# Kernel tuning notes

Measured on AMD Instinct MI355X. Metric: run time of the kernel, lower is better.

Reference implementation:

```python
import jax, jax.numpy as jnp
import numpy as np
from jax.ops import segment_sum


def gcn_conv(x, edge_index, W, b):
    """PyG GCNConv: add self-loops, symmetric D^-1/2 (A+I) D^-1/2 normalization,
    then aggregate normalized messages at target nodes. edge_weight=None -> ones."""
    N = x.shape[0]
    loops = jnp.arange(N, dtype=edge_index.dtype)
    row = jnp.concatenate([edge_index[0], loops])  # source nodes
    col = jnp.concatenate([edge_index[1], loops])  # target nodes
    w = jnp.ones(row.shape[0], dtype=x.dtype)
    deg = segment_sum(w, col, num_segments=N)
    dinv = jnp.where(deg > 0, jax.lax.rsqrt(deg), 0.0)
    norm = dinv[row] * dinv[col]                    # [E+N]
    xw = x @ W                                      # dense transform [N, out]
    msg = xw[row] * norm[:, None]                   # gather + scale [E+N, out]
    out = segment_sum(msg, col, num_segments=N)     # scatter-add at targets
    return out + b


def setup_inputs() -> dict:
    key = jax.random.key(0)
    k1, k2, k3, k4 = jax.random.split(key, 4)
    N, E, nhid, nfeat = 50000, 800000, 256, 128
    x = jax.random.normal(k1, (N, nhid), dtype=jnp.float32)
    edge_index = jax.random.randint(k2, (2, E), 0, N, dtype=jnp.int64)
    W1 = jax.random.normal(k3, (nhid, nhid), dtype=jnp.float32) * (1.0 / np.sqrt(nhid))
    b1 = jnp.zeros((nhid,), dtype=jnp.float32)
    W2 = jax.random.normal(k4, (nhid, nfeat), dtype=jnp.float32) * (1.0 / np.sqrt(nhid))
    b2 = jnp.zeros((nfeat,), dtype=jnp.float32)
    return {"x": x, "edge_index": edge_index, "W1": W1, "b1": b1, "W2": W2, "b2": b2}


def reference(x, edge_index, W1, b1, W2, b2):
    h = jax.nn.relu(gcn_conv(x, edge_index, W1, b1))
    # dropout is identity in eval mode (deterministic reference)
    return gcn_conv(h, edge_index, W2, b2)
```

## Files before the change

### kernel.cpp

```cpp
#include <hip/hip_runtime.h>
#include <math.h>


typedef _Float16 h8 __attribute__((ext_vector_type(8)));
typedef float    f32x4 __attribute__((ext_vector_type(4)));

#define CAP 64

__global__ void k_zero(int* __restrict__ deg, int* __restrict__ govf, int N) {
    int i = blockIdx.x * blockDim.x + threadIdx.x;
    if (i < N) deg[i] = 0;
    if (i == 0) *govf = 0;
}

template<bool A32>
__device__ __forceinline__ void gemm_body(
    const float* __restrict__ X32, const _Float16* __restrict__ X16,
    const _Float16* __restrict__ Wt, _Float16* __restrict__ Y,
    int M, int K, int NC, int bx, int by)
{
    __shared__ _Float16 As[128][40];
    __shared__ _Float16 Bs[128][40];

    const int bn = bx * 128;
    const int bm = by * 128;
    const int tid = threadIdx.x;
    const int w = tid >> 6, l = tid & 63;
    const int wm = (w >> 1) * 64, wn = (w & 1) * 64;
    const int lr = l & 15, lg = l >> 4;

    const int arow = tid >> 2, acol = (tid & 3) * 8;
    const int xrow = tid >> 1, xcol = (tid & 1) * 16;

    f32x4 acc[4][4];
    #pragma unroll
    for (int i = 0; i < 4; i++)
        #pragma unroll
        for (int j = 0; j < 4; j++)
            acc[i][j] = (f32x4){0.f, 0.f, 0.f, 0.f};

    float4 pf0, pf1, pf2, pf3;
    h8 pa0, pa1;
    h8 pb0, pb1;

    auto loadA = [&](int k0) {
        if (A32) {
            int gm0 = bm + arow;      if (gm0 >= M) gm0 = M - 1;
            int gm1 = bm + 64 + arow; if (gm1 >= M) gm1 = M - 1;
            pf0 = *reinterpret_cast<const float4*>(&X32[(long)gm0 * K + k0 + acol]);
            pf1 = *reinterpret_cast<const float4*>(&X32[(long)gm0 * K + k0 + acol + 4]);
            pf2 = *reinterpret_cast<const float4*>(&X32[(long)gm1 * K + k0 + acol]);
            pf3 = *reinterpret_cast<const float4*>(&X32[(long)gm1 * K + k0 + acol + 4]);
        } else {
            int gm = bm + xrow; if (gm >= M) gm = M - 1;
            pa0 = *reinterpret_cast<const h8*>(&X16[(long)gm * K + k0 + xcol]);
            pa1 = *reinterpret_cast<const h8*>(&X16[(long)gm * K + k0 + xcol + 8]);
        }
    };
    auto loadB = [&](int k0) {
        pb0 = *reinterpret_cast<const h8*>(&Wt[(long)(bn + xrow) * K + k0 + xcol]);
        pb1 = *reinterpret_cast<const h8*>(&Wt[(long)(bn + xrow) * K + k0 + xcol + 8]);
    };

    loadA(0); loadB(0);
    for (int k0 = 0; k0 < K; k0 += 32) {
        if (A32) {
            h8 h0, h1;
            h0[0] = (_Float16)pf0.x; h0[1] = (_Float16)pf0.y;
            h0[2] = (_Float16)pf0.z; h0[3] = (_Float16)pf0.w;
            h0[4] = (_Float16)pf1.x; h0[5] = (_Float16)pf1.y;
            h0[6] = (_Float16)pf1.z; h0[7] = (_Float16)pf1.w;
            h1[0] = (_Float16)pf2.x; h1[1] = (_Float16)pf2.y;
            h1[2] = (_Float16)pf2.z; h1[3] = (_Float16)pf2.w;
            h1[4] = (_Float16)pf3.x; h1[5] = (_Float16)pf3.y;
            h1[6] = (_Float16)pf3.z; h1[7] = (_Float16)pf3.w;
            *reinterpret_cast<h8*>(&As[arow][acol]) = h0;
            *reinterpret_cast<h8*>(&As[64 + arow][acol]) = h1;
        } else {
            *reinterpret_cast<h8*>(&As[xrow][xcol]) = pa0;
            *reinterpret_cast<h8*>(&As[xrow][xcol + 8]) = pa1;
        }
        *reinterpret_cast<h8*>(&Bs[xrow][xcol]) = pb0;
        *reinterpret_cast<h8*>(&Bs[xrow][xcol + 8]) = pb1;
        __syncthreads();

        if (k0 + 32 < K) { loadA(k0 + 32); loadB(k0 + 32); }

        h8 a[4], b[4];
        #pragma unroll
        for (int i = 0; i < 4; i++)
            a[i] = *reinterpret_cast<const h8*>(&As[wm + i * 16 + lr][lg * 8]);
        #pragma unroll
        for (int j = 0; j < 4; j++)
            b[j] = *reinterpret_cast<const h8*>(&Bs[wn + j * 16 + lr][lg * 8]);
        #pragma unroll
        for (int i = 0; i < 4; i++)
            #pragma unroll
            for (int j = 0; j < 4; j++)
                acc[i][j] = __builtin_amdgcn_mfma_f32_16x16x32_f16(
                    a[i], b[j], acc[i][j], 0, 0, 0);
        __syncthreads();
    }

    #pragma unroll
    for (int i = 0; i < 4; i++) {
        #pragma unroll
        for (int r = 0; r < 4; r++) {
            int gm = bm + wm + i * 16 + lg * 4 + r;
            if (gm < M) {
                #pragma unroll
                for (int j = 0; j < 4; j++)
                    Y[(long)gm * NC + bn + wn + j * 16 + lr] =
                        (_Float16)acc[i][j][r];
            }
        }
    }
}

__global__ __launch_bounds__(256) void k_count_prep(
    const int* __restrict__ col, int E, int* __restrict__ deg, int* __restrict__ rank,
    int ncb,
    const float* __restrict__ W1, const float* __restrict__ W2,
    _Float16* __restrict__ wt1, _Float16* __restrict__ wt2,
    int K, int n1, int n2)
{
    if ((int)blockIdx.x < ncb) {
        int i = blockIdx.x * blockDim.x + threadIdx.x;
        int s = ncb * blockDim.x;
        for (int e = i; e < E; e += s) rank[e] = atomicAdd(&deg[col[e]], 1);
        return;
    }
    int i = (blockIdx.x - ncb) * blockDim.x + threadIdx.x;
    int c1 = K * n1;
    if (i < c1) {
        int k = i / n1, n = i % n1;
        wt1[(long)n * K + k] = (_Float16)W1[i];
    } else if (i < c1 + K * n2) {
        int j = i - c1;
        int k = j / n2, n = j % n2;
        wt2[(long)n * K + k] = (_Float16)W2[j];
    }
}

__global__ __launch_bounds__(256) void k_gemm_fill(
    const float* __restrict__ X32, const _Float16* __restrict__ Wt,
    _Float16* __restrict__ Y, int M, int K, int NC, int ngb, int gx,
    const int* __restrict__ row, const int* __restrict__ col,
    const int* __restrict__ rank, int E,
    const int* __restrict__ deg, float* __restrict__ dinv, int N,
    int* __restrict__ srcidx, int2* __restrict__ ovf, int* __restrict__ govf,
    int zb)
{
    if ((int)blockIdx.x < ngb) {
        int gb = blockIdx.x;
        gemm_body<true>(X32, nullptr, Wt, Y, M, K, NC, gb % gx, gb / gx);
        return;
    }
    if ((int)blockIdx.x < ngb + zb) {
        int i = (blockIdx.x - ngb) * blockDim.x + threadIdx.x;
        if (i < N) dinv[i] = rsqrtf(1.f + (float)deg[i]);
        return;
    }
    int g = (blockIdx.x - ngb - zb) * blockDim.x + threadIdx.x;
    int nthreads = (gridDim.x - ngb - zb) * blockDim.x;
    if ((E & 3) == 0) {
        int G4 = E >> 2;
        for (int q = g; q < G4; q += nthreads) {
            int e = q << 2;
            int4 c4 = *reinterpret_cast<const int4*>(&col[e]);
            int4 r4 = *reinterpret_cast<const int4*>(&row[e]);
            int4 k4 = *reinterpret_cast<const int4*>(&rank[e]);
            if (k4.x < CAP) srcidx[c4.x * CAP + k4.x] = r4.x;
            else { int o = atomicAdd(govf, 1); ovf[o] = make_int2(r4.x, c4.x); }
            if (k4.y < CAP) srcidx[c4.y * CAP + k4.y] = r4.y;
            else { int o = atomicAdd(govf, 1); ovf[o] = make_int2(r4.y, c4.y); }
            if (k4.z < CAP) srcidx[c4.z * CAP + k4.z] = r4.z;
            else { int o = atomicAdd(govf, 1); ovf[o] = make_int2(r4.z, c4.z); }
            if (k4.w < CAP) srcidx[c4.w * CAP + k4.w] = r4.w;
            else { int o = atomicAdd(govf, 1); ovf[o] = make_int2(r4.w, c4.w); }
        }
    } else {
        for (int e = g; e < E; e += nthreads) {
            int c = col[e], r = row[e], k = rank[e];
            if (k < CAP) srcidx[c * CAP + k] = r;
            else { int o = atomicAdd(govf, 1); ovf[o] = make_int2(r, c); }
        }
    }
}

__global__ __launch_bounds__(256) void k_gemm16(
    const _Float16* __restrict__ X16, const _Float16* __restrict__ Wt,
    _Float16* __restrict__ Y, int M, int K, int NC)
{
    gemm_body<false>(nullptr, X16, Wt, Y, M, K, NC, blockIdx.x, blockIdx.y);
}

template<bool F16OUT, bool RELU>
__global__ __launch_bounds__(256) void k_agg(
    const int* __restrict__ deg, const float* __restrict__ dinv,
    const int* __restrict__ srcidx,
    const int2* __restrict__ ovf, const int* __restrict__ govf,
    const _Float16* __restrict__ Y, const float* __restrict__ bias,
    int N, int FT, int fo,
    float* __restrict__ out32, _Float16* __restrict__ out16)
{
    int node = blockIdx.x * 4 + (threadIdx.x >> 6);
    if (node >= N) return;
    int lane = threadIdx.x & 63;
    int sub = lane >> 4;
    int fl  = lane & 15;
    const int fcol = fo + fl * 8;

    float dc = dinv[node];
    int cnt = min(deg[node], CAP);
    const int beg = node * CAP;

    float acc[8];
    if (sub == 0) {
        h8 v = *reinterpret_cast<const h8*>(&Y[(long)node * FT + fcol]);
        #pragma unroll
        for (int j = 0; j < 8; j++) acc[j] = dc * (float)v[j];
    } else {
        #pragma unroll
        for (int j = 0; j < 8; j++) acc[j] = 0.f;
    }

    int base16 = cnt & ~15;
    for (int i = sub * 4; i < base16; i += 16) {
        int4 r4 = *reinterpret_cast<const int4*>(&srcidx[beg + i]);
        float d0 = dinv[r4.x], d1 = dinv[r4.y], d2 = dinv[r4.z], d3 = dinv[r4.w];
        h8 v0 = *reinterpret_cast<const h8*>(&Y[(long)r4.x * FT + fcol]);
        h8 v1 = *reinterpret_cast<const h8*>(&Y[(long)r4.y * FT + fcol]);
        h8 v2 = *reinterpret_cast<const h8*>(&Y[(long)r4.z * FT + fcol]);
        h8 v3 = *reinterpret_cast<const h8*>(&Y[(long)r4.w * FT + fcol]);
        #pragma unroll
        for (int j = 0; j < 8; j++) {
            acc[j] = fmaf(d0, (float)v0[j], acc[j]);
            acc[j] = fmaf(d1, (float)v1[j], acc[j]);
            acc[j] = fmaf(d2, (float)v2[j], acc[j]);
            acc[j] = fmaf(d3, (float)v3[j], acc[j]);
        }
    }
    for (int i = base16 + sub; i < cnt; i += 4) {
        int r = srcidx[beg + i];
        float d = dinv[r];
        h8 v = *reinterpret_cast<const h8*>(&Y[(long)r * FT + fcol]);
        #pragma unroll
        for (int j = 0; j < 8; j++) acc[j] = fmaf(d, (float)v[j], acc[j]);
    }
    {
        int no = *govf;
        for (int t = sub; t < no; t += 4) {
            int2 pr = ovf[t];
            if (pr.y == node) {
                float d = dinv[pr.x];
                h8 v = *reinterpret_cast<const h8*>(&Y[(long)pr.x * FT + fcol]);
                #pragma unroll
                for (int j = 0; j < 8; j++) acc[j] = fmaf(d, (float)v[j], acc[j]);
            }
        }
    }

    #pragma unroll
    for (int m = 16; m < 64; m <<= 1)
        #pragma unroll
        for (int j = 0; j < 8; j++)
            acc[j] += __shfl_xor(acc[j], m, 64);

    const float4* b4 = reinterpret_cast<const float4*>(&bias[fcol]);
    float4 blo = b4[0], bhi = b4[1];
    float r8[8];
    r8[0] = fmaf(dc, acc[0], blo.x); r8[1] = fmaf(dc, acc[1], blo.y);
    r8[2] = fmaf(dc, acc[2], blo.z); r8[3] = fmaf(dc, acc[3], blo.w);
    r8[4] = fmaf(dc, acc[4], bhi.x); r8[5] = fmaf(dc, acc[5], bhi.y);
    r8[6] = fmaf(dc, acc[6], bhi.z); r8[7] = fmaf(dc, acc[7], bhi.w);
    if (RELU) {
        #pragma unroll
        for (int j = 0; j < 8; j++) r8[j] = fmaxf(r8[j], 0.f);
    }

    long base = (long)node * FT + fcol;
    if (F16OUT) {
        if (sub == 0) {
            h8 o;
            #pragma unroll
            for (int j = 0; j < 8; j++) o[j] = (_Float16)r8[j];
            *reinterpret_cast<h8*>(&out16[base]) = o;
        }
    } else {
        if (sub == 0) {
            *reinterpret_cast<float4*>(&out32[base]) =
                make_float4(r8[0], r8[1], r8[2], r8[3]);
        } else if (sub == 1) {
            *reinterpret_cast<float4*>(&out32[base + 4]) =
                make_float4(r8[4], r8[5], r8[6], r8[7]);
        }
    }
}

extern "C" void kernel_launch(void* const* d_in, const int* in_sizes, int n_in,
                              void* d_out, int out_size, void* d_ws, size_t ws_size,
                              hipStream_t stream)
{
    const float* x   = (const float*)d_in[0];
    const int*   ei  = (const int*)d_in[1];
    const float* W1  = (const float*)d_in[2];
    const float* b1  = (const float*)d_in[3];
    const float* W2  = (const float*)d_in[4];
    const float* b2  = (const float*)d_in[5];

    const int nhid  = in_sizes[3];
    const int nfeat = in_sizes[5];
    const int N     = in_sizes[0] / nhid;
    const int E     = in_sizes[1] / 2;

    const int* row = ei;
    const int* col = ei + E;

    size_t cur = 0;
    auto alloc = [&](size_t bytes) {
        void* p = (char*)d_ws + cur;
        cur += (bytes + 255) & ~(size_t)255;
        return p;
    };
    int*       deg_i  = (int*)alloc((size_t)N * 4);
    int*       govf   = (int*)alloc(256);
    float*     dinv   = (float*)alloc((size_t)N * 4);
    int*       rank   = (int*)alloc((size_t)E * 4);
    int*       srcidx = (int*)alloc((size_t)N * CAP * 4);
    int2*      ovf    = (int2*)alloc((size_t)E * 8);
    _Float16*  wt1    = (_Float16*)alloc((size_t)nhid * nhid * 2);
    _Float16*  wt2    = (_Float16*)alloc((size_t)nhid * nfeat * 2);
    _Float16*  y16    = (_Float16*)alloc((size_t)N * nhid * 2);
    _Float16*  h16    = (_Float16*)alloc((size_t)N * nhid * 2);
    _Float16*  y2     = (_Float16*)alloc((size_t)N * nfeat * 2);
    float*     out    = (float*)d_out;
    (void)ws_size; (void)n_in; (void)out_size;

    const int T = 256;
    const int zb = (N + T - 1) / T;
    const int gx = nhid / 128;
    const int gy = (N + 127) / 128;

    k_zero<<<zb, T, 0, stream>>>(deg_i, govf, N);

    {
        const int ncb = 1024;
        int pb = (nhid * (nhid + nfeat) + T - 1) / T;
        k_count_prep<<<ncb + pb, T, 0, stream>>>(
            col, E, deg_i, rank, ncb, W1, W2, wt1, wt2, nhid, nhid, nfeat);
    }

    {
        int ngb = gx * gy;
        k_gemm_fill<<<ngb + zb + 1024, T, 0, stream>>>(
            x, wt1, y16, N, nhid, nhid, ngb, gx,
            row, col, rank, E, deg_i, dinv, N, srcidx, ovf, govf, zb);
    }

    {
        int nblk = (N + 3) / 4;
        k_agg<true, true><<<nblk, T, 0, stream>>>(
            deg_i, dinv, srcidx, ovf, govf, y16, b1, N, nhid, 0, nullptr, h16);
        k_agg<true, true><<<nblk, T, 0, stream>>>(
            deg_i, dinv, srcidx, ovf, govf, y16, b1, N, nhid, 128, nullptr, h16);
    }

    {
        dim3 grid(nfeat / 128, (N + 127) / 128);
        k_gemm16<<<grid, T, 0, stream>>>(h16, wt2, y2, N, nhid, nfeat);
    }
    {
        int nblk = (N + 3) / 4;
        k_agg<false, false><<<nblk, T, 0, stream>>>(
            deg_i, dinv, srcidx, ovf, govf, y2, b2, N, nfeat, 0, out, nullptr);
    }
}
```

Before: 184.7 us.

## Fuse degree counting into edge fill and drop rank buffer

The atomic degree count and the scatter of source indices into per-node slots now happen in one pass inside the GEMM-combined kernel, so the separate counting pass and the rank array (written and then reread) are gone. Weight conversion is folded into the zeroing kernel, and dinv moves to its own small kernel after the fill. This saves one pass over the column array plus E*4 bytes of rank writes and reads. The cost is one extra kernel launch for dinv, and the fill blocks now wait on atomic return values while they share the GPU with the GEMM.

Result: slower. 189.4 us (+2.5%).

```diff
diff --git a/kernel.cpp b/kernel.cpp
--- a/kernel.cpp
+++ b/kernel.cpp
@@ -7,10 +7,27 @@
 
 #define CAP 64
 
-__global__ void k_zero(int* __restrict__ deg, int* __restrict__ govf, int N) {
-    int i = blockIdx.x * blockDim.x + threadIdx.x;
-    if (i < N) deg[i] = 0;
-    if (i == 0) *govf = 0;
+__global__ void k_zero_prep(int* __restrict__ deg, int* __restrict__ govf, int N,
+                            const float* __restrict__ W1, const float* __restrict__ W2,
+                            _Float16* __restrict__ wt1, _Float16* __restrict__ wt2,
+                            int K, int n1, int n2, int zb)
+{
+    if ((int)blockIdx.x < zb) {
+        int i = blockIdx.x * blockDim.x + threadIdx.x;
+        if (i < N) deg[i] = 0;
+        if (i == 0) *govf = 0;
+    } else {
+        int i = (blockIdx.x - zb) * blockDim.x + threadIdx.x;
+        int c1 = K * n1;
+        if (i < c1) {
+            int k = i / n1, n = i % n1;
+            wt1[(long)n * K + k] = (_Float16)W1[i];
+        } else if (i < c1 + K * n2) {
+            int j = i - c1;
+            int k = j / n2, n = j % n2;
+            wt2[(long)n * K + k] = (_Float16)W2[j];
+        }
+    }
 }
 
 template<bool A32>
@@ -117,75 +134,52 @@
     }
 }
 
-__global__ __launch_bounds__(256) void k_count_prep(
-    const int* __restrict__ col, int E, int* __restrict__ deg, int* __restrict__ rank,
-    int ncb,
-    const float* __restrict__ W1, const float* __restrict__ W2,
-    _Float16* __restrict__ wt1, _Float16* __restrict__ wt2,
-    int K, int n1, int n2)
-{
-    if ((int)blockIdx.x < ncb) {
-        int i = blockIdx.x * blockDim.x + threadIdx.x;
-        int s = ncb * blockDim.x;
-        for (int e = i; e < E; e += s) rank[e] = atomicAdd(&deg[col[e]], 1);
-        return;
-    }
-    int i = (blockIdx.x - ncb) * blockDim.x + threadIdx.x;
-    int c1 = K * n1;
-    if (i < c1) {
-        int k = i / n1, n = i % n1;
-        wt1[(long)n * K + k] = (_Float16)W1[i];
-    } else if (i < c1 + K * n2) {
-        int j = i - c1;
-        int k = j / n2, n = j % n2;
-        wt2[(long)n * K + k] = (_Float16)W2[j];
-    }
-}
-
-__global__ __launch_bounds__(256) void k_gemm_fill(
+__global__ __launch_bounds__(256) void k_gemm_cfg(
     const float* __restrict__ X32, const _Float16* __restrict__ Wt,
     _Float16* __restrict__ Y, int M, int K, int NC, int ngb, int gx,
-    const int* __restrict__ row, const int* __restrict__ col,
-    const int* __restrict__ rank, int E,
-    const int* __restrict__ deg, float* __restrict__ dinv, int N,
-    int* __restrict__ srcidx, int2* __restrict__ ovf, int* __restrict__ govf,
-    int zb)
+    const int* __restrict__ row, const int* __restrict__ col, int E,
+    int* __restrict__ deg, int* __restrict__ srcidx,
+    int2* __restrict__ ovf, int* __restrict__ govf)
 {
     if ((int)blockIdx.x < ngb) {
         int gb = blockIdx.x;
         gemm_body<true>(X32, nullptr, Wt, Y, M, K, NC, gb % gx, gb / gx);
         return;
     }
-    if ((int)blockIdx.x < ngb + zb) {
-        int i = (blockIdx.x - ngb) * blockDim.x + threadIdx.x;
-        if (i < N) dinv[i] = rsqrtf(1.f + (float)deg[i]);
-        return;
-    }
-    int g = (blockIdx.x - ngb - zb) * blockDim.x + threadIdx.x;
-    int nthreads = (gridDim.x - ngb - zb) * blockDim.x;
+    int g = (blockIdx.x - ngb) * blockDim.x + threadIdx.x;
+    int nthreads = (gridDim.x - ngb) * blockDim.x;
     if ((E & 3) == 0) {
         int G4 = E >> 2;
         for (int q = g; q < G4; q += nthreads) {
             int e = q << 2;
             int4 c4 = *reinterpret_cast<const int4*>(&col[e]);
             int4 r4 = *reinterpret_cast<const int4*>(&row[e]);
-            int4 k4 = *reinterpret_cast<const int4*>(&rank[e]);
-            if (k4.x < CAP) srcidx[c4.x * CAP + k4.x] = r4.x;
+            int k0 = atomicAdd(&deg[c4.x], 1);
+            int k1 = atomicAdd(&deg[c4.y], 1);
+            int k2 = atomicAdd(&deg[c4.z], 1);
+            int k3 = atomicAdd(&deg[c4.w], 1);
+            if (k0 < CAP) srcidx[c4.x * CAP + k0] = r4.x;
             else { int o = atomicAdd(govf, 1); ovf[o] = make_int2(r4.x, c4.x); }
-            if (k4.y < CAP) srcidx[c4.y * CAP + k4.y] = r4.y;
+            if (k1 < CAP) srcidx[c4.y * CAP + k1] = r4.y;
             else { int o = atomicAdd(govf, 1); ovf[o] = make_int2(r4.y, c4.y); }
-            if (k4.z < CAP) srcidx[c4.z * CAP + k4.z] = r4.z;
+            if (k2 < CAP) srcidx[c4.z * CAP + k2] = r4.z;
             else { int o = atomicAdd(govf, 1); ovf[o] = make_int2(r4.z, c4.z); }
-            if (k4.w < CAP) srcidx[c4.w * CAP + k4.w] = r4.w;
+            if (k3 < CAP) srcidx[c4.w * CAP + k3] = r4.w;
             else { int o = atomicAdd(govf, 1); ovf[o] = make_int2(r4.w, c4.w); }
         }
     } else {
         for (int e = g; e < E; e += nthreads) {
-            int c = col[e], r = row[e], k = rank[e];
+            int c = col[e], r = row[e];
+            int k = atomicAdd(&deg[c], 1);
             if (k < CAP) srcidx[c * CAP + k] = r;
             else { int o = atomicAdd(govf, 1); ovf[o] = make_int2(r, c); }
         }
     }
+}
+
+__global__ void k_dinv(const int* __restrict__ deg, float* __restrict__ dinv, int N) {
+    int i = blockIdx.x * blockDim.x + threadIdx.x;
+    if (i < N) dinv[i] = rsqrtf(1.f + (float)deg[i]);
 }
 
 __global__ __launch_bounds__(256) void k_gemm16(
@@ -326,7 +320,6 @@
     int*       deg_i  = (int*)alloc((size_t)N * 4);
     int*       govf   = (int*)alloc(256);
     float*     dinv   = (float*)alloc((size_t)N * 4);
-    int*       rank   = (int*)alloc((size_t)E * 4);
     int*       srcidx = (int*)alloc((size_t)N * CAP * 4);
     int2*      ovf    = (int2*)alloc((size_t)E * 8);
     _Float16*  wt1    = (_Float16*)alloc((size_t)nhid * nhid * 2);
@@ -342,21 +335,20 @@
     const int gx = nhid / 128;
     const int gy = (N + 127) / 128;
 
-    k_zero<<<zb, T, 0, stream>>>(deg_i, govf, N);
-
-    {
-        const int ncb = 1024;
+    {
         int pb = (nhid * (nhid + nfeat) + T - 1) / T;
-        k_count_prep<<<ncb + pb, T, 0, stream>>>(
-            col, E, deg_i, rank, ncb, W1, W2, wt1, wt2, nhid, nhid, nfeat);
+        k_zero_prep<<<zb + pb, T, 0, stream>>>(deg_i, govf, N, W1, W2, wt1, wt2,
+                                               nhid, nhid, nfeat, zb);
     }
 
     {
         int ngb = gx * gy;
-        k_gemm_fill<<<ngb + zb + 1024, T, 0, stream>>>(
+        k_gemm_cfg<<<ngb + 1024, T, 0, stream>>>(
             x, wt1, y16, N, nhid, nhid, ngb, gx,
-            row, col, rank, E, deg_i, dinv, N, srcidx, ovf, govf, zb);
-    }
+            row, col, E, deg_i, srcidx, ovf, govf);
+    }
+
+    k_dinv<<<zb, T, 0, stream>>>(deg_i, dinv, N);
 
     {
         int nblk = (N + 3) / 4;
```

## Use full-width 128x256 tiles with 512-thread blocks for first GEMM

Applied to the files above, without the earlier changes.

The first GEMM now gives each 512-thread block a 128x256 output tile covering all output columns, instead of two 128x128 blocks per row tile. Each fp32 row of X is then read and converted to fp16 only once rather than twice, which halves A-side global traffic and conversion work. The fused dinv and fill sections are re-indexed for the 512-thread block size, and the second GEMM is inlined as its own kernel. In exchange, per-block LDS and register use rise, which may lower occupancy, and the fill work runs with the larger block geometry.

New measurement: 177.0 us, median of 2. 4.1% less time.

```diff
diff --git a/kernel.cpp b/kernel.cpp
--- a/kernel.cpp
+++ b/kernel.cpp
@@ -11,110 +11,6 @@
     int i = blockIdx.x * blockDim.x + threadIdx.x;
     if (i < N) deg[i] = 0;
     if (i == 0) *govf = 0;
-}
-
-template<bool A32>
-__device__ __forceinline__ void gemm_body(
-    const float* __restrict__ X32, const _Float16* __restrict__ X16,
-    const _Float16* __restrict__ Wt, _Float16* __restrict__ Y,
-    int M, int K, int NC, int bx, int by)
-{
-    __shared__ _Float16 As[128][40];
-    __shared__ _Float16 Bs[128][40];
-
-    const int bn = bx * 128;
-    const int bm = by * 128;
-    const int tid = threadIdx.x;
-    const int w = tid >> 6, l = tid & 63;
-    const int wm = (w >> 1) * 64, wn = (w & 1) * 64;
-    const int lr = l & 15, lg = l >> 4;
-
-    const int arow = tid >> 2, acol = (tid & 3) * 8;
-    const int xrow = tid >> 1, xcol = (tid & 1) * 16;
-
-    f32x4 acc[4][4];
-    #pragma unroll
-    for (int i = 0; i < 4; i++)
-        #pragma unroll
-        for (int j = 0; j < 4; j++)
-            acc[i][j] = (f32x4){0.f, 0.f, 0.f, 0.f};
-
-    float4 pf0, pf1, pf2, pf3;
-    h8 pa0, pa1;
-    h8 pb0, pb1;
-
-    auto loadA = [&](int k0) {
-        if (A32) {
-            int gm0 = bm + arow;      if (gm0 >= M) gm0 = M - 1;
-            int gm1 = bm + 64 + arow; if (gm1 >= M) gm1 = M - 1;
-            pf0 = *reinterpret_cast<const float4*>(&X32[(long)gm0 * K + k0 + acol]);
-            pf1 = *reinterpret_cast<const float4*>(&X32[(long)gm0 * K + k0 + acol + 4]);
-            pf2 = *reinterpret_cast<const float4*>(&X32[(long)gm1 * K + k0 + acol]);
-            pf3 = *reinterpret_cast<const float4*>(&X32[(long)gm1 * K + k0 + acol + 4]);
-        } else {
-            int gm = bm + xrow; if (gm >= M) gm = M - 1;
-            pa0 = *reinterpret_cast<const h8*>(&X16[(long)gm * K + k0 + xcol]);
-            pa1 = *reinterpret_cast<const h8*>(&X16[(long)gm * K + k0 + xcol + 8]);
-        }
-    };
-    auto loadB = [&](int k0) {
-        pb0 = *reinterpret_cast<const h8*>(&Wt[(long)(bn + xrow) * K + k0 + xcol]);
-        pb1 = *reinterpret_cast<const h8*>(&Wt[(long)(bn + xrow) * K + k0 + xcol + 8]);
-    };
-
-    loadA(0); loadB(0);
-    for (int k0 = 0; k0 < K; k0 += 32) {
-        if (A32) {
-            h8 h0, h1;
-            h0[0] = (_Float16)pf0.x; h0[1] = (_Float16)pf0.y;
-            h0[2] = (_Float16)pf0.z; h0[3] = (_Float16)pf0.w;
-            h0[4] = (_Float16)pf1.x; h0[5] = (_Float16)pf1.y;
-            h0[6] = (_Float16)pf1.z; h0[7] = (_Float16)pf1.w;
-            h1[0] = (_Float16)pf2.x; h1[1] = (_Float16)pf2.y;
-            h1[2] = (_Float16)pf2.z; h1[3] = (_Float16)pf2.w;
-            h1[4] = (_Float16)pf3.x; h1[5] = (_Float16)pf3.y;
-            h1[6] = (_Float16)pf3.z; h1[7] = (_Float16)pf3.w;
-            *reinterpret_cast<h8*>(&As[arow][acol]) = h0;
-            *reinterpret_cast<h8*>(&As[64 + arow][acol]) = h1;
-        } else {
-            *reinterpret_cast<h8*>(&As[xrow][xcol]) = pa0;
-            *reinterpret_cast<h8*>(&As[xrow][xcol + 8]) = pa1;
-        }
-        *reinterpret_cast<h8*>(&Bs[xrow][xcol]) = pb0;
-        *reinterpret_cast<h8*>(&Bs[xrow][xcol + 8]) = pb1;
-        __syncthreads();
-
-        if (k0 + 32 < K) { loadA(k0 + 32); loadB(k0 + 32); }
-
-        h8 a[4], b[4];
-        #pragma unroll
-        for (int i = 0; i < 4; i++)
-            a[i] = *reinterpret_cast<const h8*>(&As[wm + i * 16 + lr][lg * 8]);
-        #pragma unroll
-        for (int j = 0; j < 4; j++)
-            b[j] = *reinterpret_cast<const h8*>(&Bs[wn + j * 16 + lr][lg * 8]);
-        #pragma unroll
-        for (int i = 0; i < 4; i++)
-            #pragma unroll
-            for (int j = 0; j < 4; j++)
-                acc[i][j] = __builtin_amdgcn_mfma_f32_16x16x32_f16(
-                    a[i], b[j], acc[i][j], 0, 0, 0);
-        __syncthreads();
-    }
-
-    #pragma unroll
-    for (int i = 0; i < 4; i++) {
-        #pragma unroll
-        for (int r = 0; r < 4; r++) {
-            int gm = bm + wm + i * 16 + lg * 4 + r;
-            if (gm < M) {
-                #pragma unroll
-                for (int j = 0; j < 4; j++)
-                    Y[(long)gm * NC + bn + wn + j * 16 + lr] =
-                        (_Float16)acc[i][j][r];
-            }
-        }
-    }
 }
 
 __global__ __launch_bounds__(256) void k_count_prep(
@@ -142,27 +38,107 @@
     }
 }
 
-__global__ __launch_bounds__(256) void k_gemm_fill(
+__device__ __forceinline__ void gemm1_body(
     const float* __restrict__ X32, const _Float16* __restrict__ Wt,
-    _Float16* __restrict__ Y, int M, int K, int NC, int ngb, int gx,
+    _Float16* __restrict__ Y, int M, int K, int by)
+{
+    __shared__ _Float16 As[128][40];
+    __shared__ _Float16 Bs[256][40];
+
+    const int bm = by * 128;
+    const int tid = threadIdx.x;
+    const int w = tid >> 6, l = tid & 63;
+    const int wm = (w >> 2) * 64, wn = (w & 3) * 64;
+    const int lr = l & 15, lg = l >> 4;
+
+    const int arow = tid >> 2, acol = (tid & 3) * 8;
+    const int brow = tid >> 1, bcol = (tid & 1) * 16;
+
+    f32x4 acc[4][4];
+    #pragma unroll
+    for (int i = 0; i < 4; i++)
+        #pragma unroll
+        for (int j = 0; j < 4; j++)
+            acc[i][j] = (f32x4){0.f, 0.f, 0.f, 0.f};
+
+    float4 pf0, pf1;
+    h8 pb0, pb1;
+
+    auto loadA = [&](int k0) {
+        int gm = bm + arow; if (gm >= M) gm = M - 1;
+        pf0 = *reinterpret_cast<const float4*>(&X32[(long)gm * K + k0 + acol]);
+        pf1 = *reinterpret_cast<const float4*>(&X32[(long)gm * K + k0 + acol + 4]);
+    };
+    auto loadB = [&](int k0) {
+        pb0 = *reinterpret_cast<const h8*>(&Wt[(long)brow * K + k0 + bcol]);
+        pb1 = *reinterpret_cast<const h8*>(&Wt[(long)brow * K + k0 + bcol + 8]);
+    };
+
+    loadA(0); loadB(0);
+    for (int k0 = 0; k0 < K; k0 += 32) {
+        h8 hv;
+        hv[0] = (_Float16)pf0.x; hv[1] = (_Float16)pf0.y;
+        hv[2] = (_Float16)pf0.z; hv[3] = (_Float16)pf0.w;
+        hv[4] = (_Float16)pf1.x; hv[5] = (_Float16)pf1.y;
+        hv[6] = (_Float16)pf1.z; hv[7] = (_Float16)pf1.w;
+        *reinterpret_cast<h8*>(&As[arow][acol]) = hv;
+        *reinterpret_cast<h8*>(&Bs[brow][bcol]) = pb0;
+        *reinterpret_cast<h8*>(&Bs[brow][bcol + 8]) = pb1;
+        __syncthreads();
+
+        if (k0 + 32 < K) { loadA(k0 + 32); loadB(k0 + 32); }
+
+        h8 a[4], b[4];
+        #pragma unroll
+        for (int i = 0; i < 4; i++)
+            a[i] = *reinterpret_cast<const h8*>(&As[wm + i * 16 + lr][lg * 8]);
+        #pragma unroll
+        for (int j = 0; j < 4; j++)
+            b[j] = *reinterpret_cast<const h8*>(&Bs[wn + j * 16 + lr][lg * 8]);
+        #pragma unroll
+        for (int i = 0; i < 4; i++)
+            #pragma unroll
+            for (int j = 0; j < 4; j++)
+                acc[i][j] = __builtin_amdgcn_mfma_f32_16x16x32_f16(
+                    a[i], b[j], acc[i][j], 0, 0, 0);
+        __syncthreads();
+    }
+
+    #pragma unroll
+    for (int i = 0; i < 4; i++) {
+        #pragma unroll
+        for (int r = 0; r < 4; r++) {
+            int gm = bm + wm + i * 16 + lg * 4 + r;
+            if (gm < M) {
+                #pragma unroll
+                for (int j = 0; j < 4; j++)
+                    Y[(long)gm * 256 + wn + j * 16 + lr] =
+                        (_Float16)acc[i][j][r];
+            }
+        }
+    }
+}
+
+__global__ __launch_bounds__(512) void k_gemm_fill(
+    const float* __restrict__ X32, const _Float16* __restrict__ Wt,
+    _Float16* __restrict__ Y, int M, int K, int ngb,
     const int* __restrict__ row, const int* __restrict__ col,
     const int* __restrict__ rank, int E,
     const int* __restrict__ deg, float* __restrict__ dinv, int N,
     int* __restrict__ srcidx, int2* __restrict__ ovf, int* __restrict__ govf,
-    int zb)
+    int zb5)
 {
     if ((int)blockIdx.x < ngb) {
-        int gb = blockIdx.x;
-        gemm_body<true>(X32, nullptr, Wt, Y, M, K, NC, gb % gx, gb / gx);
+        gemm1_body(X32, Wt, Y, M, K, blockIdx.x);
         return;
     }
-    if ((int)blockIdx.x < ngb + zb) {
+    if ((int)blockIdx.x < ngb + zb5) {
         int i = (blockIdx.x - ngb) * blockDim.x + threadIdx.x;
         if (i < N) dinv[i] = rsqrtf(1.f + (float)deg[i]);
         return;
     }
-    int g = (blockIdx.x - ngb - zb) * blockDim.x + threadIdx.x;
-    int nthreads = (gridDim.x - ngb - zb) * blockDim.x;
+    int g = (blockIdx.x - ngb - zb5) * blockDim.x + threadIdx.x;
+    int nthreads = (gridDim.x - ngb - zb5) * blockDim.x;
     if ((E & 3) == 0) {
         int G4 = E >> 2;
         for (int q = g; q < G4; q += nthreads) {
@@ -192,7 +168,74 @@
     const _Float16* __restrict__ X16, const _Float16* __restrict__ Wt,
     _Float16* __restrict__ Y, int M, int K, int NC)
 {
-    gemm_body<false>(nullptr, X16, Wt, Y, M, K, NC, blockIdx.x, blockIdx.y);
+    __shared__ _Float16 As[128][40];
+    __shared__ _Float16 Bs[128][40];
+
+    const int bn = blockIdx.x * 128;
+    const int bm = blockIdx.y * 128;
+    const int tid = threadIdx.x;
+    const int w = tid >> 6, l = tid & 63;
+    const int wm = (w >> 1) * 64, wn = (w & 1) * 64;
+    const int lr = l & 15, lg = l >> 4;
+    const int xrow = tid >> 1, xcol = (tid & 1) * 16;
+
+    f32x4 acc[4][4];
+    #pragma unroll
+    for (int i = 0; i < 4; i++)
+        #pragma unroll
+        for (int j = 0; j < 4; j++)
+            acc[i][j] = (f32x4){0.f, 0.f, 0.f, 0.f};
+
+    h8 pa0, pa1, pb0, pb1;
+    auto loadA = [&](int k0) {
+        int gm = bm + xrow; if (gm >= M) gm = M - 1;
+        pa0 = *reinterpret_cast<const h8*>(&X16[(long)gm * K + k0 + xcol]);
+        pa1 = *reinterpret_cast<const h8*>(&X16[(long)gm * K + k0 + xcol + 8]);
+    };
+    auto loadB = [&](int k0) {
+        pb0 = *reinterpret_cast<const h8*>(&Wt[(long)(bn + xrow) * K + k0 + xcol]);
+        pb1 = *reinterpret_cast<const h8*>(&Wt[(long)(bn + xrow) * K + k0 + xcol + 8]);
+    };
+
+    loadA(0); loadB(0);
+    for (int k0 = 0; k0 < K; k0 += 32) {
+        *reinterpret_cast<h8*>(&As[xrow][xcol]) = pa0;
+        *reinterpret_cast<h8*>(&As[xrow][xcol + 8]) = pa1;
+        *reinterpret_cast<h8*>(&Bs[xrow][xcol]) = pb0;
+        *reinterpret_cast<h8*>(&Bs[xrow][xcol + 8]) = pb1;
+        __syncthreads();
+
+        if (k0 + 32 < K) { loadA(k0 + 32); loadB(k0 + 32); }
+
+        h8 a[4], b[4];
+        #pragma unroll
+        for (int i = 0; i < 4; i++)
+            a[i] = *reinterpret_cast<const h8*>(&As[wm + i * 16 + lr][lg * 8]);
+        #pragma unroll
+        for (int j = 0; j < 4; j++)
+            b[j] = *reinterpret_cast<const h8*>(&Bs[wn + j * 16 + lr][lg * 8]);
+        #pragma unroll
+        for (int i = 0; i < 4; i++)
+            #pragma unroll
+            for (int j = 0; j < 4; j++)
+                acc[i][j] = __builtin_amdgcn_mfma_f32_16x16x32_f16(
+                    a[i], b[j], acc[i][j], 0, 0, 0);
+        __syncthreads();
+    }
+
+    #pragma unroll
+    for (int i = 0; i < 4; i++) {
+        #pragma unroll
+        for (int r = 0; r < 4; r++) {
+            int gm = bm + wm + i * 16 + lg * 4 + r;
+            if (gm < M) {
+                #pragma unroll
+                for (int j = 0; j < 4; j++)
+                    Y[(long)gm * NC + bn + wn + j * 16 + lr] =
+                        (_Float16)acc[i][j][r];
+            }
+        }
+    }
 }
 
 template<bool F16OUT, bool RELU>
@@ -338,9 +381,9 @@
     (void)ws_size; (void)n_in; (void)out_size;
 
     const int T = 256;
-    const int zb = (N + T - 1) / T;
-    const int gx = nhid / 128;
-    const int gy = (N + 127) / 128;
+    const int zb  = (N + T - 1) / T;
+    const int zb5 = (N + 511) / 512;
+    const int gy  = (N + 127) / 128;
 
     k_zero<<<zb, T, 0, stream>>>(deg_i, govf, N);
 
@@ -352,10 +395,10 @@
     }
 
     {
-        int ngb = gx * gy;
-        k_gemm_fill<<<ngb + zb + 1024, T, 0, stream>>>(
-            x, wt1, y16, N, nhid, nhid, ngb, gx,
-            row, col, rank, E, deg_i, dinv, N, srcidx, ovf, govf, zb);
+        int ngb = gy;
+        k_gemm_fill<<<ngb + zb5 + 1024, 512, 0, stream>>>(
+            x, wt1, y16, N, nhid, ngb,
+            row, col, rank, E, deg_i, dinv, N, srcidx, ovf, govf, zb5);
     }
 
     {
```
